# Kernel tuning notes

Hardware: AMD Instinct MI355X
Metric: run time of the kernel (lower is better)

The kernel has to match this reference:

```python
import jax, jax.numpy as jnp
import numpy as np

D_MODEL = 1024
N_HEADS = 16
D_K = D_MODEL // N_HEADS


def setup_inputs() -> dict:
    key = jax.random.key(0)
    ks = jax.random.split(key, 9)
    s = 1.0 / np.sqrt(D_MODEL)
    inp = {
        "x": jax.random.normal(ks[0], (4, 2048, D_MODEL), dtype=jnp.float32),
        "wq": jax.random.normal(ks[1], (D_MODEL, D_MODEL), dtype=jnp.float32) * s,
        "bq": jax.random.normal(ks[2], (D_MODEL,), dtype=jnp.float32) * 0.01,
        "wk": jax.random.normal(ks[3], (D_MODEL, D_MODEL), dtype=jnp.float32) * s,
        "bk": jax.random.normal(ks[4], (D_MODEL,), dtype=jnp.float32) * 0.01,
        "wv": jax.random.normal(ks[5], (D_MODEL, D_MODEL), dtype=jnp.float32) * s,
        "bv": jax.random.normal(ks[6], (D_MODEL,), dtype=jnp.float32) * 0.01,
        "wo": jax.random.normal(ks[7], (D_MODEL, D_MODEL), dtype=jnp.float32) * s,
        "bo": jax.random.normal(ks[8], (D_MODEL,), dtype=jnp.float32) * 0.01,
    }
    return inp


def reference(x, wq, bq, wk, bk, wv, bv, wo, bo):
    B, S, _ = x.shape
    # QKV projections (weights stored [in, out] so y = x @ w + b)
    q = (x @ wq + bq).reshape(B, S, N_HEADS, D_K).transpose(0, 2, 1, 3)  # [B,H,S,Dk]
    k = (x @ wk + bk).reshape(B, S, N_HEADS, D_K).transpose(0, 2, 1, 3)
    v = (x @ wv + bv).reshape(B, S, N_HEADS, D_K).transpose(0, 2, 1, 3)
    scale = 1.0 / jnp.sqrt(jnp.asarray(D_K, dtype=x.dtype))
    scores = jnp.einsum("bhqd,bhkd->bhqk", q, k) * scale  # [B,H,S,S]
    attn = jax.nn.softmax(scores, axis=-1)
    out = jnp.einsum("bhqk,bhkd->bhqd", attn, v)  # [B,H,S,Dk]
    out = out.transpose(0, 2, 1, 3).reshape(B, S, D_MODEL)
    return out @ wo + bo
```

## Files before the change

kernel.cpp:

```cpp
#include <hip/hip_runtime.h>

#define D_MODEL 1024
#define NH 16
#define DK 64
#define BB 4
#define SS 2048
#define MROWS (BB*SS)

typedef __attribute__((ext_vector_type(4))) float f32x4;
typedef __attribute__((ext_vector_type(16))) float f32x16;
typedef __attribute__((ext_vector_type(8))) short short8;
typedef __attribute__((ext_vector_type(4))) float float4v;
typedef __attribute__((ext_vector_type(2))) unsigned u32x2;

typedef const __attribute__((address_space(1))) void* gas_t;
typedef __attribute__((address_space(3))) void* las_t;

static __device__ __forceinline__ ushort f2bf(float f) {
  union { float f; unsigned u; } v; v.f = f;
  unsigned r = 0x7fffu + ((v.u >> 16) & 1u);
  return (ushort)((v.u + r) >> 16);
}

#define VM_WAIT(N)                                              \
  do {                                                          \
    asm volatile("s_waitcnt vmcnt(" #N ")" ::: "memory");       \
    __builtin_amdgcn_sched_barrier(0);                          \
  } while (0)

__global__ __launch_bounds__(256) void convert_x_k(const float* __restrict__ x,
                                                   ushort* __restrict__ xb) {
  int i = blockIdx.x * 256 + threadIdx.x;
  float4v v = ((const float4v*)x)[i];
  ushort4 o;
  o.x = f2bf(v.x); o.y = f2bf(v.y); o.z = f2bf(v.z); o.w = f2bf(v.w);
  ((ushort4*)xb)[i] = o;
}

__global__ __launch_bounds__(256) void convert_wt4_k(const float* __restrict__ w0,
                                                     const float* __restrict__ w1,
                                                     const float* __restrict__ w2,
                                                     const float* __restrict__ w3,
                                                     ushort* __restrict__ t0,
                                                     ushort* __restrict__ t1,
                                                     ushort* __restrict__ t2,
                                                     ushort* __restrict__ t3) {
  __shared__ float tile[64][65];
  const float* w; ushort* wt;
  switch (blockIdx.z) {
    case 0: w = w0; wt = t0; break;
    case 1: w = w1; wt = t1; break;
    case 2: w = w2; wt = t2; break;
    default: w = w3; wt = t3; break;
  }
  int bx = blockIdx.x, by = blockIdx.y;
  int tx = threadIdx.x & 63, ty = threadIdx.x >> 6;
#pragma unroll
  for (int i = 0; i < 16; ++i) {
    int r = i * 4 + ty;
    tile[r][tx] = w[(size_t)(by * 64 + r) * D_MODEL + bx * 64 + tx];
  }
  __syncthreads();
#pragma unroll
  for (int i = 0; i < 16; ++i) {
    int r = i * 4 + ty;
    wt[(size_t)(bx * 64 + r) * D_MODEL + by * 64 + tx] = f2bf(tile[tx][r]);
  }
}

__global__ __launch_bounds__(256) void gemm_qkv_k(const ushort* __restrict__ A,
                                                  const ushort* __restrict__ Bt,
                                                  const float* __restrict__ bq,
                                                  const float* __restrict__ bk,
                                                  const float* __restrict__ bv,
                                                  ushort* __restrict__ Qw,
                                                  ushort* __restrict__ Kw,
                                                  ushort* __restrict__ Vw,
                                                  float qscale) {
  const int K = D_MODEL;
  __shared__ __align__(16) ushort As[2][128 * 32];
  __shared__ __align__(16) ushort Bs[2][128 * 32];
  const int nbn = 24;
  int bid = blockIdx.x;
  int wg = (bid & 7) * 192 + (bid >> 3);
  int bm = wg / nbn, bn = wg % nbn;
  const int t = threadIdx.x;
  const int l = t & 63;
  const int w = t >> 6;
  const int g = l >> 4, q = l & 15;
  const int wr = w >> 1, wc = w & 1;

  f32x4 acc[4][4];
#pragma unroll
  for (int m = 0; m < 4; ++m)
#pragma unroll
    for (int n = 0; n < 4; ++n) acc[m][n] = f32x4{0.f, 0.f, 0.f, 0.f};

  const ushort* Ab = A + (size_t)bm * 128 * K;
  const ushort* Bb = Bt + (size_t)bn * 128 * K;

#define GSTAGE(BUF, KT)                                                                      \
  do {                                                                                       \
    _Pragma("unroll") for (int i_ = 0; i_ < 2; ++i_) {                                       \
      int c_ = i_ * 256 + t;                                                                 \
      __builtin_amdgcn_global_load_lds((gas_t)(Ab + (size_t)(c_ >> 2) * K + (KT) + (c_ & 3) * 8), \
                                       (las_t)(As[BUF] + c_ * 8), 16, 0, 0);                 \
      __builtin_amdgcn_global_load_lds((gas_t)(Bb + (size_t)(c_ >> 2) * K + (KT) + (c_ & 3) * 8), \
                                       (las_t)(Bs[BUF] + c_ * 8), 16, 0, 0);                 \
    }                                                                                        \
  } while (0)

  GSTAGE(0, 0);
  int cur = 0;

  for (int kt = 0; kt < K; kt += 32) {
    if (kt + 32 < K) {
      GSTAGE(cur ^ 1, kt + 32);
      VM_WAIT(4);
    } else {
      VM_WAIT(0);
    }
    __builtin_amdgcn_s_barrier();
    __builtin_amdgcn_sched_barrier(0);
    short8 af[4], bf[4];
#pragma unroll
    for (int m = 0; m < 4; ++m)
      af[m] = *(const short8*)(As[cur] + (wr * 64 + m * 16 + q) * 32 + g * 8);
#pragma unroll
    for (int n = 0; n < 4; ++n)
      bf[n] = *(const short8*)(Bs[cur] + (wc * 64 + n * 16 + q) * 32 + g * 8);
#pragma unroll
    for (int m = 0; m < 4; ++m)
#pragma unroll
      for (int n = 0; n < 4; ++n)
        acc[m][n] = __builtin_amdgcn_mfma_f32_16x16x32_bf16(af[m], bf[n], acc[m][n], 0, 0, 0);
    __builtin_amdgcn_sched_barrier(0);
    __builtin_amdgcn_s_barrier();
    cur ^= 1;
  }
#undef GSTAGE

  const int sec = (bn * 128) >> 10;
  const float* bias = sec == 0 ? bq : (sec == 1 ? bk : bv);
  const float scale = sec == 0 ? qscale : 1.0f;
  ushort* dst = sec == 0 ? Qw : Kw;
  const int rbase0 = bm * 128 + wr * 64 + g * 4;
  const int cbase = (bn * 128 + wc * 64 + q) & 1023;
#pragma unroll
  for (int m = 0; m < 4; ++m) {
    int r0 = rbase0 + m * 16;
#pragma unroll
    for (int n = 0; n < 4; ++n) {
      int c = cbase + n * 16;
      float bv_ = bias[c];
      if (sec == 2) {
        ushort4 pk;
        pk.x = f2bf(acc[m][n][0] + bv_);
        pk.y = f2bf(acc[m][n][1] + bv_);
        pk.z = f2bf(acc[m][n][2] + bv_);
        pk.w = f2bf(acc[m][n][3] + bv_);
        size_t off = (((size_t)((r0 >> 11) * NH + (c >> 6))) * DK + (c & 63)) * (size_t)SS + (r0 & (SS - 1));
        *(ushort4*)(Vw + off) = pk;
      } else {
#pragma unroll
        for (int j = 0; j < 4; ++j) {
          int r = r0 + j;
          float v = (acc[m][n][j] + bv_) * scale;
          size_t off = (((size_t)((r >> 11) * NH + (c >> 6))) * SS + (r & (SS - 1))) * DK + (c & 63);
          dst[off] = f2bf(v);
        }
      }
    }
  }
}

__global__ __launch_bounds__(256) void gemm_out_k(const ushort* __restrict__ A,
                                                  const ushort* __restrict__ Bt,
                                                  const float* __restrict__ bias,
                                                  float* __restrict__ outp) {
  const int K = D_MODEL;
  __shared__ __align__(16) ushort As[2][128 * 32];
  __shared__ __align__(16) ushort Bs[2][128 * 32];
  const int nbn = 8;
  int bid = blockIdx.x;
  int wg = (bid & 7) * 64 + (bid >> 3);
  int bm = wg / nbn, bn = wg % nbn;
  const int t = threadIdx.x;
  const int l = t & 63;
  const int w = t >> 6;
  const int g = l >> 4, q = l & 15;
  const int wr = w >> 1, wc = w & 1;

  f32x4 acc[4][4];
#pragma unroll
  for (int m = 0; m < 4; ++m)
#pragma unroll
    for (int n = 0; n < 4; ++n) acc[m][n] = f32x4{0.f, 0.f, 0.f, 0.f};

  const ushort* Ab = A + (size_t)bm * 128 * K;
  const ushort* Bb = Bt + (size_t)bn * 128 * K;

#define GSTAGE(BUF, KT)                                                                      \
  do {                                                                                       \
    _Pragma("unroll") for (int i_ = 0; i_ < 2; ++i_) {                                       \
      int c_ = i_ * 256 + t;                                                                 \
      __builtin_amdgcn_global_load_lds((gas_t)(Ab + (size_t)(c_ >> 2) * K + (KT) + (c_ & 3) * 8), \
                                       (las_t)(As[BUF] + c_ * 8), 16, 0, 0);                 \
      __builtin_amdgcn_global_load_lds((gas_t)(Bb + (size_t)(c_ >> 2) * K + (KT) + (c_ & 3) * 8), \
                                       (las_t)(Bs[BUF] + c_ * 8), 16, 0, 0);                 \
    }                                                                                        \
  } while (0)

  GSTAGE(0, 0);
  int cur = 0;

  for (int kt = 0; kt < K; kt += 32) {
    if (kt + 32 < K) {
      GSTAGE(cur ^ 1, kt + 32);
      VM_WAIT(4);
    } else {
      VM_WAIT(0);
    }
    __builtin_amdgcn_s_barrier();
    __builtin_amdgcn_sched_barrier(0);
    short8 af[4], bf[4];
#pragma unroll
    for (int m = 0; m < 4; ++m)
      af[m] = *(const short8*)(As[cur] + (wr * 64 + m * 16 + q) * 32 + g * 8);
#pragma unroll
    for (int n = 0; n < 4; ++n)
      bf[n] = *(const short8*)(Bs[cur] + (wc * 64 + n * 16 + q) * 32 + g * 8);
#pragma unroll
    for (int m = 0; m < 4; ++m)
#pragma unroll
      for (int n = 0; n < 4; ++n)
        acc[m][n] = __builtin_amdgcn_mfma_f32_16x16x32_bf16(af[m], bf[n], acc[m][n], 0, 0, 0);
    __builtin_amdgcn_sched_barrier(0);
    __builtin_amdgcn_s_barrier();
    cur ^= 1;
  }
#undef GSTAGE

  const int rbase0 = bm * 128 + wr * 64 + g * 4;
  const int cbase = bn * 128 + wc * 64 + q;
#pragma unroll
  for (int m = 0; m < 4; ++m) {
    int r0 = rbase0 + m * 16;
#pragma unroll
    for (int n = 0; n < 4; ++n) {
      int c = cbase + n * 16;
      float bv = bias[c];
#pragma unroll
      for (int j = 0; j < 4; ++j)
        outp[(size_t)(r0 + j) * D_MODEL + c] = acc[m][n][j] + bv;
    }
  }
}

__global__ __launch_bounds__(256, 4) void attn_k(const ushort* __restrict__ Qm,
                                                 const ushort* __restrict__ Km,
                                                 const ushort* __restrict__ Vm,
                                                 ushort* __restrict__ Ob) {
  __shared__ __align__(16) ushort Ks[2][64 * 64];
  __shared__ __align__(16) ushort Vs[2][64 * 64];
  const int bid = blockIdx.x;
  const int logical = (bid & 7) * 128 + (bid >> 3);
  const int bh = logical >> 4;
  const int qblk = logical & 15;
  const int t = threadIdx.x, l = t & 63, w = t >> 6;
  const int q = l & 31, h = l >> 5;
  const int qsw = q & 7;

  const ushort* Qb = Qm + ((size_t)bh * SS + qblk * 128 + w * 32) * DK;
  const ushort* Kb = Km + (size_t)bh * SS * DK;
  const ushort* Vb = Vm + (size_t)bh * DK * SS;

  short8 qf[4];
#pragma unroll
  for (int ks = 0; ks < 4; ++ks)
    qf[ks] = *(const short8*)(Qb + q * DK + ks * 16 + h * 8);

  f32x16 oacc[2];
#pragma unroll
  for (int d = 0; d < 2; ++d)
#pragma unroll
    for (int r = 0; r < 16; ++r) oacc[d][r] = 0.f;
  float lrun = 0.f;

  const int cg = (l & 7) ^ ((l >> 3) & 7);

#define STAGE(B, KT)                                                                        \
  do {                                                                                      \
    _Pragma("unroll") for (int i_ = 0; i_ < 2; ++i_) {                                      \
      int row_ = w * 16 + i_ * 8 + (l >> 3);                                                \
      __builtin_amdgcn_global_load_lds((gas_t)(Kb + (size_t)((KT) + row_) * DK + cg * 8),   \
                                       (las_t)(Ks[B] + (w * 16 + i_ * 8) * 64 + l * 8),     \
                                       16, 0, 0);                                           \
      __builtin_amdgcn_global_load_lds((gas_t)(Vb + (size_t)row_ * SS + (KT) + cg * 8),     \
                                       (las_t)(Vs[B] + (w * 16 + i_ * 8) * 64 + l * 8),     \
                                       16, 0, 0);                                           \
    }                                                                                       \
  } while (0)

  STAGE(0, 0);
  int cur = 0;

  for (int kt = 0; kt < SS; kt += 64) {
    __syncthreads();
    if (kt + 64 < SS) STAGE(cur ^ 1, kt + 64);

    const ushort* Kc = Ks[cur];
    const ushort* Vc = Vs[cur];

    f32x16 sc[2];
#pragma unroll
    for (int n = 0; n < 2; ++n)
#pragma unroll
      for (int r = 0; r < 16; ++r) sc[n][r] = 0.f;

    __builtin_amdgcn_s_setprio(1);
#pragma unroll
    for (int ks = 0; ks < 4; ++ks) {
      int ch = ((ks * 2 + h) ^ qsw) * 8;
      short8 kf0 = *(const short8*)(Kc + q * 64 + ch);
      short8 kf1 = *(const short8*)(Kc + (32 + q) * 64 + ch);
      sc[0] = __builtin_amdgcn_mfma_f32_32x32x16_bf16(kf0, qf[ks], sc[0], 0, 0, 0);
      sc[1] = __builtin_amdgcn_mfma_f32_32x32x16_bf16(kf1, qf[ks], sc[1], 0, 0, 0);
    }
    __builtin_amdgcn_s_setprio(0);

#pragma unroll
    for (int n = 0; n < 2; ++n)
#pragma unroll
      for (int r = 0; r < 16; ++r) sc[n][r] = __builtin_amdgcn_exp2f(sc[n][r]);

    float s8[8];
#pragma unroll
    for (int i = 0; i < 8; ++i)
      s8[i] = (sc[0][i] + sc[0][i + 8]) + (sc[1][i] + sc[1][i + 8]);
#pragma unroll
    for (int i = 0; i < 4; ++i) s8[i] += s8[i + 4];
    lrun += (s8[0] + s8[1]) + (s8[2] + s8[3]);

    short8 pf[4];
#pragma unroll
    for (int n = 0; n < 2; ++n) {
      unsigned wv[8];
#pragma unroll
      for (int Qd = 0; Qd < 4; ++Qd) {
        unsigned w0, w1;
        asm("v_cvt_pk_bf16_f32 %0, %1, %2" : "=v"(w0) : "v"(sc[n][Qd * 4 + 0]), "v"(sc[n][Qd * 4 + 1]));
        asm("v_cvt_pk_bf16_f32 %0, %1, %2" : "=v"(w1) : "v"(sc[n][Qd * 4 + 2]), "v"(sc[n][Qd * 4 + 3]));
        wv[Qd * 2] = w0; wv[Qd * 2 + 1] = w1;
      }
#pragma unroll
      for (int m = 0; m < 2; ++m) {
        u32x2 r0 = __builtin_amdgcn_permlane32_swap(wv[(2 * m) * 2 + 0], wv[(2 * m + 1) * 2 + 0], false, false);
        u32x2 r1 = __builtin_amdgcn_permlane32_swap(wv[(2 * m) * 2 + 1], wv[(2 * m + 1) * 2 + 1], false, false);
        union { unsigned u[4]; short8 s; } fu;
        fu.u[0] = r0[0]; fu.u[1] = r1[0]; fu.u[2] = r0[1]; fu.u[3] = r1[1];
        pf[n * 2 + m] = fu.s;
      }
    }

    __builtin_amdgcn_s_setprio(1);
#pragma unroll
    for (int kvb = 0; kvb < 4; ++kvb) {
      int ch = ((kvb * 2 + h) ^ qsw) * 8;
      short8 vf0 = *(const short8*)(Vc + q * 64 + ch);
      short8 vf1 = *(const short8*)(Vc + (32 + q) * 64 + ch);
      oacc[0] = __builtin_amdgcn_mfma_f32_32x32x16_bf16(vf0, pf[kvb], oacc[0], 0, 0, 0);
      oacc[1] = __builtin_amdgcn_mfma_f32_32x32x16_bf16(vf1, pf[kvb], oacc[1], 0, 0, 0);
    }
    __builtin_amdgcn_s_setprio(0);
    cur ^= 1;
  }
#undef STAGE

  const int b_ = bh >> 4, h_ = bh & 15;
  float lt = lrun;
  lt += __shfl_xor(lt, 32);
  float inv = 1.0f / lt;
  const int srow = qblk * 128 + w * 32 + q;
#pragma unroll
  for (int d = 0; d < 2; ++d)
#pragma unroll
    for (int rq = 0; rq < 4; ++rq) {
      ushort4 pk;
      pk.x = f2bf(oacc[d][rq * 4 + 0] * inv);
      pk.y = f2bf(oacc[d][rq * 4 + 1] * inv);
      pk.z = f2bf(oacc[d][rq * 4 + 2] * inv);
      pk.w = f2bf(oacc[d][rq * 4 + 3] * inv);
      size_t off = ((size_t)b_ * SS + srow) * D_MODEL + h_ * 64 + d * 32 + rq * 8 + h * 4;
      *(ushort4*)(Ob + off) = pk;
    }
}

extern "C" void kernel_launch(void* const* d_in, const int* in_sizes, int n_in,
                              void* d_out, int out_size, void* d_ws, size_t ws_size,
                              hipStream_t stream) {
  (void)in_sizes; (void)n_in; (void)out_size; (void)ws_size;
  const float* x  = (const float*)d_in[0];
  const float* wq = (const float*)d_in[1];
  const float* bq = (const float*)d_in[2];
  const float* wk = (const float*)d_in[3];
  const float* bk = (const float*)d_in[4];
  const float* wv = (const float*)d_in[5];
  const float* bv = (const float*)d_in[6];
  const float* wo = (const float*)d_in[7];
  const float* bo = (const float*)d_in[8];

  char* ws = (char*)d_ws;
  ushort* xb    = (ushort*)(ws);
  ushort* wqkvt = (ushort*)(ws + 16777216);
  ushort* wot   = (ushort*)(ws + 16777216 + 6291456);
  ushort* Qw    = (ushort*)(ws + 16777216 + 6291456 + 2097152);
  ushort* Kw    = (ushort*)(ws + 16777216 + 6291456 + 2097152 + 16777216);
  ushort* Vw    = (ushort*)(ws + 16777216 + 6291456 + 2097152 + 2 * 16777216);
  ushort* Obw   = xb;

  convert_x_k<<<MROWS * D_MODEL / 4 / 256, 256, 0, stream>>>(x, xb);
  convert_wt4_k<<<dim3(16, 16, 4), 256, 0, stream>>>(
      wq, wk, wv, wo, wqkvt, wqkvt + 1024 * 1024, wqkvt + 2 * 1024 * 1024, wot);

  gemm_qkv_k<<<1536, 256, 0, stream>>>(xb, wqkvt, bq, bk, bv, Qw, Kw, Vw,
                                       0.125f * 1.44269504088896f);

  attn_k<<<1024, 256, 0, stream>>>(Qw, Kw, Vw, Obw);

  gemm_out_k<<<512, 256, 0, stream>>>(Obw, wot, bo, (float*)d_out);
}
```

Before: 197.2 us.

## Enlarge QKV GEMM tile to 256x128x64 with triple-buffered swizzled LDS

Reworks the QKV projection GEMM to use 512-thread blocks computing 256x128 output tiles with a K-step of 64. LDS stages grow to three buffers so global loads run two stages ahead, and an XOR swizzle on the LDS column chunks is meant to avoid bank conflicts on the wider rows. MFMA issue is split into two halves, each with explicit lgkmcnt waits and raised wave priority. The aim is more data reuse per load and better latency hiding, at the cost of much more LDS per block (about 144 KB), which may limit blocks per CU.

```diff
diff --git a/kernel.cpp b/kernel.cpp
--- a/kernel.cpp
+++ b/kernel.cpp
@@ -25,6 +25,12 @@
 #define VM_WAIT(N)                                              \
   do {                                                          \
     asm volatile("s_waitcnt vmcnt(" #N ")" ::: "memory");       \
+    __builtin_amdgcn_sched_barrier(0);                          \
+  } while (0)
+
+#define LGKM0()                                                 \
+  do {                                                          \
+    asm volatile("s_waitcnt lgkmcnt(0)" ::: "memory");          \
     __builtin_amdgcn_sched_barrier(0);                          \
   } while (0)
 
@@ -68,7 +74,7 @@
   }
 }
 
-__global__ __launch_bounds__(256) void gemm_qkv_k(const ushort* __restrict__ A,
+__global__ __launch_bounds__(512) void gemm_qkv_k(const ushort* __restrict__ A,
                                                   const ushort* __restrict__ Bt,
                                                   const float* __restrict__ bq,
                                                   const float* __restrict__ bk,
@@ -78,17 +84,18 @@
                                                   ushort* __restrict__ Vw,
                                                   float qscale) {
   const int K = D_MODEL;
-  __shared__ __align__(16) ushort As[2][128 * 32];
-  __shared__ __align__(16) ushort Bs[2][128 * 32];
+  __shared__ __align__(16) ushort As[3][256 * 64];
+  __shared__ __align__(16) ushort Bs[3][128 * 64];
   const int nbn = 24;
   int bid = blockIdx.x;
-  int wg = (bid & 7) * 192 + (bid >> 3);
+  int wg = (bid & 7) * 96 + (bid >> 3);
   int bm = wg / nbn, bn = wg % nbn;
   const int t = threadIdx.x;
   const int l = t & 63;
   const int w = t >> 6;
   const int g = l >> 4, q = l & 15;
   const int wr = w >> 1, wc = w & 1;
+  const int qs = q & 7;
 
   f32x4 acc[4][4];
 #pragma unroll
@@ -96,47 +103,75 @@
 #pragma unroll
     for (int n = 0; n < 4; ++n) acc[m][n] = f32x4{0.f, 0.f, 0.f, 0.f};
 
-  const ushort* Ab = A + (size_t)bm * 128 * K;
+  const ushort* Ab = A + (size_t)bm * 256 * K;
   const ushort* Bb = Bt + (size_t)bn * 128 * K;
 
-#define GSTAGE(BUF, KT)                                                                      \
-  do {                                                                                       \
-    _Pragma("unroll") for (int i_ = 0; i_ < 2; ++i_) {                                       \
-      int c_ = i_ * 256 + t;                                                                 \
-      __builtin_amdgcn_global_load_lds((gas_t)(Ab + (size_t)(c_ >> 2) * K + (KT) + (c_ & 3) * 8), \
-                                       (las_t)(As[BUF] + c_ * 8), 16, 0, 0);                 \
-      __builtin_amdgcn_global_load_lds((gas_t)(Bb + (size_t)(c_ >> 2) * K + (KT) + (c_ & 3) * 8), \
-                                       (las_t)(Bs[BUF] + c_ * 8), 16, 0, 0);                 \
-    }                                                                                        \
+#define GSTAGE(BUF, KT)                                                                       \
+  do {                                                                                        \
+    _Pragma("unroll") for (int i_ = 0; i_ < 4; ++i_) {                                        \
+      int c_ = i_ * 512 + t;                                                                  \
+      int r_ = c_ >> 3;                                                                       \
+      int gc_ = (c_ & 7) ^ (r_ & 7);                                                          \
+      __builtin_amdgcn_global_load_lds((gas_t)(Ab + (size_t)r_ * K + (KT) * 64 + gc_ * 8),    \
+                                       (las_t)(&As[BUF][c_ * 8]), 16, 0, 0);                  \
+    }                                                                                         \
+    _Pragma("unroll") for (int i_ = 0; i_ < 2; ++i_) {                                        \
+      int c_ = i_ * 512 + t;                                                                  \
+      int r_ = c_ >> 3;                                                                       \
+      int gc_ = (c_ & 7) ^ (r_ & 7);                                                          \
+      __builtin_amdgcn_global_load_lds((gas_t)(Bb + (size_t)r_ * K + (KT) * 64 + gc_ * 8),    \
+                                       (las_t)(&Bs[BUF][c_ * 8]), 16, 0, 0);                  \
+    }                                                                                         \
   } while (0)
 
   GSTAGE(0, 0);
-  int cur = 0;
-
-  for (int kt = 0; kt < K; kt += 32) {
-    if (kt + 32 < K) {
-      GSTAGE(cur ^ 1, kt + 32);
-      VM_WAIT(4);
+  GSTAGE(1, 1);
+
+  for (int kt = 0; kt < 16; ++kt) {
+    if (kt + 2 < 16) {
+      GSTAGE((kt + 2) % 3, kt + 2);
+      VM_WAIT(12);
+    } else if (kt + 1 < 16) {
+      VM_WAIT(6);
     } else {
       VM_WAIT(0);
     }
     __builtin_amdgcn_s_barrier();
     __builtin_amdgcn_sched_barrier(0);
-    short8 af[4], bf[4];
-#pragma unroll
-    for (int m = 0; m < 4; ++m)
-      af[m] = *(const short8*)(As[cur] + (wr * 64 + m * 16 + q) * 32 + g * 8);
+
+    const ushort* Ac = As[kt % 3];
+    const ushort* Bc = Bs[kt % 3];
+
+    short8 bf[4][2];
 #pragma unroll
     for (int n = 0; n < 4; ++n)
-      bf[n] = *(const short8*)(Bs[cur] + (wc * 64 + n * 16 + q) * 32 + g * 8);
-#pragma unroll
-    for (int m = 0; m < 4; ++m)
-#pragma unroll
-      for (int n = 0; n < 4; ++n)
-        acc[m][n] = __builtin_amdgcn_mfma_f32_16x16x32_bf16(af[m], bf[n], acc[m][n], 0, 0, 0);
+#pragma unroll
+      for (int ks = 0; ks < 2; ++ks)
+        bf[n][ks] = *(const short8*)(Bc + (wc * 64 + n * 16 + q) * 64 + (((ks * 4 + g) ^ qs) * 8));
+
+#pragma unroll
+    for (int mh = 0; mh < 2; ++mh) {
+      short8 af[2][2];
+#pragma unroll
+      for (int m2 = 0; m2 < 2; ++m2)
+#pragma unroll
+        for (int ks = 0; ks < 2; ++ks)
+          af[m2][ks] = *(const short8*)(Ac + (wr * 64 + (mh * 2 + m2) * 16 + q) * 64 + (((ks * 4 + g) ^ qs) * 8));
+      LGKM0();
+      __builtin_amdgcn_s_setprio(1);
+#pragma unroll
+      for (int m2 = 0; m2 < 2; ++m2)
+#pragma unroll
+        for (int n = 0; n < 4; ++n)
+#pragma unroll
+          for (int ks = 0; ks < 2; ++ks)
+            acc[mh * 2 + m2][n] =
+                __builtin_amdgcn_mfma_f32_16x16x32_bf16(af[m2][ks], bf[n][ks], acc[mh * 2 + m2][n], 0, 0, 0);
+      __builtin_amdgcn_s_setprio(0);
+    }
+
     __builtin_amdgcn_sched_barrier(0);
     __builtin_amdgcn_s_barrier();
-    cur ^= 1;
   }
 #undef GSTAGE
 
@@ -144,7 +179,7 @@
   const float* bias = sec == 0 ? bq : (sec == 1 ? bk : bv);
   const float scale = sec == 0 ? qscale : 1.0f;
   ushort* dst = sec == 0 ? Qw : Kw;
-  const int rbase0 = bm * 128 + wr * 64 + g * 4;
+  const int rbase0 = bm * 256 + wr * 64 + g * 4;
   const int cbase = (bn * 128 + wc * 64 + q) & 1023;
 #pragma unroll
   for (int m = 0; m < 4; ++m) {
@@ -423,8 +458,8 @@
   convert_wt4_k<<<dim3(16, 16, 4), 256, 0, stream>>>(
       wq, wk, wv, wo, wqkvt, wqkvt + 1024 * 1024, wqkvt + 2 * 1024 * 1024, wot);
 
-  gemm_qkv_k<<<1536, 256, 0, stream>>>(xb, wqkvt, bq, bk, bv, Qw, Kw, Vw,
-                                       0.125f * 1.44269504088896f);
+  gemm_qkv_k<<<768, 512, 0, stream>>>(xb, wqkvt, bq, bk, bv, Qw, Kw, Vw,
+                                      0.125f * 1.44269504088896f);
 
   attn_k<<<1024, 256, 0, stream>>>(Qw, Kw, Vw, Obw);
 
```

Result: no change. 195.7 us (median of 2 runs) (-0.8%).

## Rewrite projection GEMMs with 256x128 tiles, triple-buffered swizzled LDS pipeline

Applied to the files above, without the earlier changes.

Both projection GEMMs now share a new core: 512-thread blocks computing 256x128 tiles with K-step 64, a three-deep LDS ring filled by global_load_lds, and an XOR swizzle to avoid bank conflicts. Global loads for stage k+2 are interleaved between MFMA sub-phases separated by barriers and lgkmcnt waits, with setprio raised around the MFMAs. The attention kernel also starts the first score MFMA from a zero vector instead of zeroing accumulators in a loop. Larger tiles give more reuse but also more LDS (about 144KB) and more registers per block, so fewer blocks fit per CU and the grid has fewer blocks.

```diff
diff --git a/kernel.cpp b/kernel.cpp
--- a/kernel.cpp
+++ b/kernel.cpp
@@ -25,6 +25,12 @@
 #define VM_WAIT(N)                                              \
   do {                                                          \
     asm volatile("s_waitcnt vmcnt(" #N ")" ::: "memory");       \
+    __builtin_amdgcn_sched_barrier(0);                          \
+  } while (0)
+
+#define LGKM0()                                                 \
+  do {                                                          \
+    asm volatile("s_waitcnt lgkmcnt(0)" ::: "memory");          \
     __builtin_amdgcn_sched_barrier(0);                          \
   } while (0)
 
@@ -68,7 +74,103 @@
   }
 }
 
-__global__ __launch_bounds__(256) void gemm_qkv_k(const ushort* __restrict__ A,
+#define GEMM_CORE(ACC, AB, BB_, KDIM)                                                         \
+  __shared__ __align__(16) ushort As[3][256 * 64];                                            \
+  __shared__ __align__(16) ushort Bs[3][128 * 64];                                            \
+  const int t = threadIdx.x;                                                                  \
+  const int l = t & 63;                                                                       \
+  const int w = t >> 6;                                                                       \
+  const int g = l >> 4, q = l & 15;                                                           \
+  const int wr = w >> 1, wc = w & 1;                                                          \
+  const int qs = q & 7;                                                                       \
+  f32x4 ACC[4][4];                                                                            \
+  _Pragma("unroll") for (int m = 0; m < 4; ++m)                                               \
+    _Pragma("unroll") for (int n = 0; n < 4; ++n) ACC[m][n] = f32x4{0.f, 0.f, 0.f, 0.f};      \
+  const int NT = (KDIM) / 64;                                                                 \
+                                                        \
+  GL_A(0, 0, 0); GL_A(0, 0, 1); GL_A(0, 0, 2); GL_A(0, 0, 3); GL_B(0, 0, 0); GL_B(0, 0, 1);  \
+  GL_A(1, 1, 0); GL_A(1, 1, 1); GL_A(1, 1, 2); GL_A(1, 1, 3); GL_B(1, 1, 0); GL_B(1, 1, 1);  \
+  VM_WAIT(6);                                                                                 \
+  __builtin_amdgcn_s_barrier();                                                               \
+  for (int kt = 0; kt < NT; ++kt) {                                                           \
+    const ushort* Ac = As[kt % 3];                                                            \
+    const ushort* Bc = Bs[kt % 3];                                                            \
+    const int sb = (kt + 2) % 3;                                                              \
+    const int stkt = kt + 2;                                                                  \
+    const bool st = stkt < NT;                                                                \
+    short8 bf0[4], bf1[4], af[2];                                                             \
+                                    \
+    _Pragma("unroll") for (int n = 0; n < 4; ++n)                                             \
+      bf0[n] = *(const short8*)(Bc + (wc * 64 + n * 16 + q) * 64 + ((g ^ qs) * 8));           \
+    af[0] = *(const short8*)(Ac + (wr * 64 + 0 + q) * 64 + ((g ^ qs) * 8));                   \
+    af[1] = *(const short8*)(Ac + (wr * 64 + 16 + q) * 64 + ((g ^ qs) * 8));                  \
+    if (st) { GL_A(sb, stkt, 0); GL_A(sb, stkt, 1); }                                         \
+    __builtin_amdgcn_s_barrier();                                                             \
+    LGKM0();                                                                                  \
+    __builtin_amdgcn_s_setprio(1);                                                            \
+    _Pragma("unroll") for (int m2 = 0; m2 < 2; ++m2)                                          \
+      _Pragma("unroll") for (int n = 0; n < 4; ++n)                                           \
+        ACC[m2][n] = __builtin_amdgcn_mfma_f32_16x16x32_bf16(af[m2], bf0[n], ACC[m2][n], 0, 0, 0); \
+    __builtin_amdgcn_s_setprio(0);                                                            \
+    __builtin_amdgcn_s_barrier();                                                             \
+                                            \
+    af[0] = *(const short8*)(Ac + (wr * 64 + 32 + q) * 64 + ((g ^ qs) * 8));                  \
+    af[1] = *(const short8*)(Ac + (wr * 64 + 48 + q) * 64 + ((g ^ qs) * 8));                  \
+    if (st) { GL_A(sb, stkt, 2); GL_A(sb, stkt, 3); }                                         \
+    __builtin_amdgcn_s_barrier();                                                             \
+    LGKM0();                                                                                  \
+    __builtin_amdgcn_s_setprio(1);                                                            \
+    _Pragma("unroll") for (int m2 = 0; m2 < 2; ++m2)                                          \
+      _Pragma("unroll") for (int n = 0; n < 4; ++n)                                           \
+        ACC[2 + m2][n] = __builtin_amdgcn_mfma_f32_16x16x32_bf16(af[m2], bf0[n], ACC[2 + m2][n], 0, 0, 0); \
+    __builtin_amdgcn_s_setprio(0);                                                            \
+    __builtin_amdgcn_s_barrier();                                                             \
+                                    \
+    _Pragma("unroll") for (int n = 0; n < 4; ++n)                                             \
+      bf1[n] = *(const short8*)(Bc + (wc * 64 + n * 16 + q) * 64 + (((4 + g) ^ qs) * 8));     \
+    af[0] = *(const short8*)(Ac + (wr * 64 + 0 + q) * 64 + (((4 + g) ^ qs) * 8));             \
+    af[1] = *(const short8*)(Ac + (wr * 64 + 16 + q) * 64 + (((4 + g) ^ qs) * 8));            \
+    if (st) { GL_B(sb, stkt, 0); GL_B(sb, stkt, 1); }                                         \
+    __builtin_amdgcn_s_barrier();                                                             \
+    LGKM0();                                                                                  \
+    __builtin_amdgcn_s_setprio(1);                                                            \
+    _Pragma("unroll") for (int m2 = 0; m2 < 2; ++m2)                                          \
+      _Pragma("unroll") for (int n = 0; n < 4; ++n)                                           \
+        ACC[m2][n] = __builtin_amdgcn_mfma_f32_16x16x32_bf16(af[m2], bf1[n], ACC[m2][n], 0, 0, 0); \
+    __builtin_amdgcn_s_setprio(0);                                                            \
+    __builtin_amdgcn_s_barrier();                                                             \
+                          \
+    af[0] = *(const short8*)(Ac + (wr * 64 + 32 + q) * 64 + (((4 + g) ^ qs) * 8));            \
+    af[1] = *(const short8*)(Ac + (wr * 64 + 48 + q) * 64 + (((4 + g) ^ qs) * 8));            \
+    __builtin_amdgcn_s_barrier();                                                             \
+    LGKM0();                                                                                  \
+    __builtin_amdgcn_s_setprio(1);                                                            \
+    _Pragma("unroll") for (int m2 = 0; m2 < 2; ++m2)                                          \
+      _Pragma("unroll") for (int n = 0; n < 4; ++n)                                           \
+        ACC[2 + m2][n] = __builtin_amdgcn_mfma_f32_16x16x32_bf16(af[m2], bf1[n], ACC[2 + m2][n], 0, 0, 0); \
+    __builtin_amdgcn_s_setprio(0);                                                            \
+    if (kt + 2 < NT) { VM_WAIT(6); } else if (kt + 1 < NT) { VM_WAIT(0); }                    \
+    __builtin_amdgcn_s_barrier();                                                             \
+  }
+
+#define GL_A(BUF, KT, I)                                                                      \
+  do {                                                                                        \
+    int c_ = (I) * 512 + threadIdx.x;                                                         \
+    int r_ = c_ >> 3;                                                                         \
+    int gc_ = (c_ & 7) ^ (r_ & 7);                                                            \
+    __builtin_amdgcn_global_load_lds((gas_t)(Ab + (size_t)r_ * D_MODEL + (KT) * 64 + gc_ * 8),\
+                                     (las_t)(&As[BUF][c_ * 8]), 16, 0, 0);                    \
+  } while (0)
+#define GL_B(BUF, KT, I)                                                                      \
+  do {                                                                                        \
+    int c_ = (I) * 512 + threadIdx.x;                                                         \
+    int r_ = c_ >> 3;                                                                         \
+    int gc_ = (c_ & 7) ^ (r_ & 7);                                                            \
+    __builtin_amdgcn_global_load_lds((gas_t)(Bb + (size_t)r_ * D_MODEL + (KT) * 64 + gc_ * 8),\
+                                     (las_t)(&Bs[BUF][c_ * 8]), 16, 0, 0);                    \
+  } while (0)
+
+__global__ __launch_bounds__(512) void gemm_qkv_k(const ushort* __restrict__ A,
                                                   const ushort* __restrict__ Bt,
                                                   const float* __restrict__ bq,
                                                   const float* __restrict__ bk,
@@ -77,74 +179,19 @@
                                                   ushort* __restrict__ Kw,
                                                   ushort* __restrict__ Vw,
                                                   float qscale) {
-  const int K = D_MODEL;
-  __shared__ __align__(16) ushort As[2][128 * 32];
-  __shared__ __align__(16) ushort Bs[2][128 * 32];
-  const int nbn = 24;
   int bid = blockIdx.x;
-  int wg = (bid & 7) * 192 + (bid >> 3);
-  int bm = wg / nbn, bn = wg % nbn;
-  const int t = threadIdx.x;
-  const int l = t & 63;
-  const int w = t >> 6;
-  const int g = l >> 4, q = l & 15;
-  const int wr = w >> 1, wc = w & 1;
-
-  f32x4 acc[4][4];
-#pragma unroll
-  for (int m = 0; m < 4; ++m)
-#pragma unroll
-    for (int n = 0; n < 4; ++n) acc[m][n] = f32x4{0.f, 0.f, 0.f, 0.f};
-
-  const ushort* Ab = A + (size_t)bm * 128 * K;
-  const ushort* Bb = Bt + (size_t)bn * 128 * K;
-
-#define GSTAGE(BUF, KT)                                                                      \
-  do {                                                                                       \
-    _Pragma("unroll") for (int i_ = 0; i_ < 2; ++i_) {                                       \
-      int c_ = i_ * 256 + t;                                                                 \
-      __builtin_amdgcn_global_load_lds((gas_t)(Ab + (size_t)(c_ >> 2) * K + (KT) + (c_ & 3) * 8), \
-                                       (las_t)(As[BUF] + c_ * 8), 16, 0, 0);                 \
-      __builtin_amdgcn_global_load_lds((gas_t)(Bb + (size_t)(c_ >> 2) * K + (KT) + (c_ & 3) * 8), \
-                                       (las_t)(Bs[BUF] + c_ * 8), 16, 0, 0);                 \
-    }                                                                                        \
-  } while (0)
-
-  GSTAGE(0, 0);
-  int cur = 0;
-
-  for (int kt = 0; kt < K; kt += 32) {
-    if (kt + 32 < K) {
-      GSTAGE(cur ^ 1, kt + 32);
-      VM_WAIT(4);
-    } else {
-      VM_WAIT(0);
-    }
-    __builtin_amdgcn_s_barrier();
-    __builtin_amdgcn_sched_barrier(0);
-    short8 af[4], bf[4];
-#pragma unroll
-    for (int m = 0; m < 4; ++m)
-      af[m] = *(const short8*)(As[cur] + (wr * 64 + m * 16 + q) * 32 + g * 8);
-#pragma unroll
-    for (int n = 0; n < 4; ++n)
-      bf[n] = *(const short8*)(Bs[cur] + (wc * 64 + n * 16 + q) * 32 + g * 8);
-#pragma unroll
-    for (int m = 0; m < 4; ++m)
-#pragma unroll
-      for (int n = 0; n < 4; ++n)
-        acc[m][n] = __builtin_amdgcn_mfma_f32_16x16x32_bf16(af[m], bf[n], acc[m][n], 0, 0, 0);
-    __builtin_amdgcn_sched_barrier(0);
-    __builtin_amdgcn_s_barrier();
-    cur ^= 1;
-  }
-#undef GSTAGE
+  int wg = (bid & 7) * 96 + (bid >> 3);
+  int bm = wg & 31, bn = wg >> 5;
+  const ushort* Ab = A + (size_t)bm * 256 * D_MODEL;
+  const ushort* Bb = Bt + (size_t)bn * 128 * D_MODEL;
+
+  GEMM_CORE(acc, Ab, Bb, D_MODEL)
 
   const int sec = (bn * 128) >> 10;
   const float* bias = sec == 0 ? bq : (sec == 1 ? bk : bv);
   const float scale = sec == 0 ? qscale : 1.0f;
   ushort* dst = sec == 0 ? Qw : Kw;
-  const int rbase0 = bm * 128 + wr * 64 + g * 4;
+  const int rbase0 = bm * 256 + wr * 64 + g * 4;
   const int cbase = (bn * 128 + wc * 64 + q) & 1023;
 #pragma unroll
   for (int m = 0; m < 4; ++m) {
@@ -174,74 +221,19 @@
   }
 }
 
-__global__ __launch_bounds__(256) void gemm_out_k(const ushort* __restrict__ A,
+__global__ __launch_bounds__(512) void gemm_out_k(const ushort* __restrict__ A,
                                                   const ushort* __restrict__ Bt,
                                                   const float* __restrict__ bias,
                                                   float* __restrict__ outp) {
-  const int K = D_MODEL;
-  __shared__ __align__(16) ushort As[2][128 * 32];
-  __shared__ __align__(16) ushort Bs[2][128 * 32];
-  const int nbn = 8;
   int bid = blockIdx.x;
-  int wg = (bid & 7) * 64 + (bid >> 3);
-  int bm = wg / nbn, bn = wg % nbn;
-  const int t = threadIdx.x;
-  const int l = t & 63;
-  const int w = t >> 6;
-  const int g = l >> 4, q = l & 15;
-  const int wr = w >> 1, wc = w & 1;
-
-  f32x4 acc[4][4];
-#pragma unroll
-  for (int m = 0; m < 4; ++m)
-#pragma unroll
-    for (int n = 0; n < 4; ++n) acc[m][n] = f32x4{0.f, 0.f, 0.f, 0.f};
-
-  const ushort* Ab = A + (size_t)bm * 128 * K;
-  const ushort* Bb = Bt + (size_t)bn * 128 * K;
-
-#define GSTAGE(BUF, KT)                                                                      \
-  do {                                                                                       \
-    _Pragma("unroll") for (int i_ = 0; i_ < 2; ++i_) {                                       \
-      int c_ = i_ * 256 + t;                                                                 \
-      __builtin_amdgcn_global_load_lds((gas_t)(Ab + (size_t)(c_ >> 2) * K + (KT) + (c_ & 3) * 8), \
-                                       (las_t)(As[BUF] + c_ * 8), 16, 0, 0);                 \
-      __builtin_amdgcn_global_load_lds((gas_t)(Bb + (size_t)(c_ >> 2) * K + (KT) + (c_ & 3) * 8), \
-                                       (las_t)(Bs[BUF] + c_ * 8), 16, 0, 0);                 \
-    }                                                                                        \
-  } while (0)
-
-  GSTAGE(0, 0);
-  int cur = 0;
-
-  for (int kt = 0; kt < K; kt += 32) {
-    if (kt + 32 < K) {
-      GSTAGE(cur ^ 1, kt + 32);
-      VM_WAIT(4);
-    } else {
-      VM_WAIT(0);
-    }
-    __builtin_amdgcn_s_barrier();
-    __builtin_amdgcn_sched_barrier(0);
-    short8 af[4], bf[4];
-#pragma unroll
-    for (int m = 0; m < 4; ++m)
-      af[m] = *(const short8*)(As[cur] + (wr * 64 + m * 16 + q) * 32 + g * 8);
-#pragma unroll
-    for (int n = 0; n < 4; ++n)
-      bf[n] = *(const short8*)(Bs[cur] + (wc * 64 + n * 16 + q) * 32 + g * 8);
-#pragma unroll
-    for (int m = 0; m < 4; ++m)
-#pragma unroll
-      for (int n = 0; n < 4; ++n)
-        acc[m][n] = __builtin_amdgcn_mfma_f32_16x16x32_bf16(af[m], bf[n], acc[m][n], 0, 0, 0);
-    __builtin_amdgcn_sched_barrier(0);
-    __builtin_amdgcn_s_barrier();
-    cur ^= 1;
-  }
-#undef GSTAGE
-
-  const int rbase0 = bm * 128 + wr * 64 + g * 4;
+  int wg = (bid & 7) * 32 + (bid >> 3);
+  int bm = wg & 31, bn = wg >> 5;
+  const ushort* Ab = A + (size_t)bm * 256 * D_MODEL;
+  const ushort* Bb = Bt + (size_t)bn * 128 * D_MODEL;
+
+  GEMM_CORE(acc, Ab, Bb, D_MODEL)
+
+  const int rbase0 = bm * 256 + wr * 64 + g * 4;
   const int cbase = bn * 128 + wc * 64 + q;
 #pragma unroll
   for (int m = 0; m < 4; ++m) {
@@ -280,11 +272,13 @@
   for (int ks = 0; ks < 4; ++ks)
     qf[ks] = *(const short8*)(Qb + q * DK + ks * 16 + h * 8);
 
+  f32x16 zf;
+#pragma unroll
+  for (int r = 0; r < 16; ++r) zf[r] = 0.f;
+
   f32x16 oacc[2];
 #pragma unroll
-  for (int d = 0; d < 2; ++d)
-#pragma unroll
-    for (int r = 0; r < 16; ++r) oacc[d][r] = 0.f;
+  for (int d = 0; d < 2; ++d) oacc[d] = zf;
   float lrun = 0.f;
 
   const int cg = (l & 7) ^ ((l >> 3) & 7);
@@ -313,14 +307,16 @@
     const ushort* Vc = Vs[cur];
 
     f32x16 sc[2];
-#pragma unroll
-    for (int n = 0; n < 2; ++n)
-#pragma unroll
-      for (int r = 0; r < 16; ++r) sc[n][r] = 0.f;
-
     __builtin_amdgcn_s_setprio(1);
-#pragma unroll
-    for (int ks = 0; ks < 4; ++ks) {
+    {
+      int ch = (h ^ qsw) * 8;
+      short8 kf0 = *(const short8*)(Kc + q * 64 + ch);
+      short8 kf1 = *(const short8*)(Kc + (32 + q) * 64 + ch);
+      sc[0] = __builtin_amdgcn_mfma_f32_32x32x16_bf16(kf0, qf[0], zf, 0, 0, 0);
+      sc[1] = __builtin_amdgcn_mfma_f32_32x32x16_bf16(kf1, qf[0], zf, 0, 0, 0);
+    }
+#pragma unroll
+    for (int ks = 1; ks < 4; ++ks) {
       int ch = ((ks * 2 + h) ^ qsw) * 8;
       short8 kf0 = *(const short8*)(Kc + q * 64 + ch);
       short8 kf1 = *(const short8*)(Kc + (32 + q) * 64 + ch);
@@ -423,10 +419,10 @@
   convert_wt4_k<<<dim3(16, 16, 4), 256, 0, stream>>>(
       wq, wk, wv, wo, wqkvt, wqkvt + 1024 * 1024, wqkvt + 2 * 1024 * 1024, wot);
 
-  gemm_qkv_k<<<1536, 256, 0, stream>>>(xb, wqkvt, bq, bk, bv, Qw, Kw, Vw,
-                                       0.125f * 1.44269504088896f);
+  gemm_qkv_k<<<768, 512, 0, stream>>>(xb, wqkvt, bq, bk, bv, Qw, Kw, Vw,
+                                      0.125f * 1.44269504088896f);
 
   attn_k<<<1024, 256, 0, stream>>>(Qw, Kw, Vw, Obw);
 
-  gemm_out_k<<<512, 256, 0, stream>>>(Obw, wot, bo, (float*)d_out);
-}
+  gemm_out_k<<<256, 512, 0, stream>>>(Obw, wot, bo, (float*)d_out);
+}
```

Result: slower. 221.2 us (+12.1%).
